# Optimization experiments

Hardware: AMD Instinct MI355X
Metric: run time of the kernel (lower is better)

The kernel has to match this reference:

```python
import jax, jax.numpy as jnp
import numpy as np

B, N, H, E = 4, 256, 128, 16
EIN = 2 * H + 1 + E  # edge MLP input dim
LN_EPS = 1e-6  # flax nnx.LayerNorm default epsilon


def layer_norm(x, scale, bias):
    m = jnp.mean(x, axis=-1, keepdims=True)
    v = jnp.var(x, axis=-1, keepdims=True)
    return (x - m) * jax.lax.rsqrt(v + LN_EPS) * scale + bias


def mlp2(x, W1, b1, s, sb, W2, b2):
    # Linear -> LayerNorm -> ReLU -> Linear (dropout deterministic)
    h = jax.nn.relu(layer_norm(x @ W1 + b1, s, sb))
    return h @ W2 + b2


def setup_inputs() -> dict:
    key = jax.random.key(0)
    ks = jax.random.split(key, 24)

    def lin(k, fi, fo):
        k1, k2 = jax.random.split(k)
        W = jax.random.normal(k1, (fi, fo), jnp.float32) / np.sqrt(fi)
        b = jnp.zeros((fo,), jnp.float32)
        return W, b

    We1, be1 = lin(ks[0], EIN, H)
    We2, be2 = lin(ks[1], H, H)
    Wa, ba = lin(ks[2], EIN, 1)
    Wn1, bn1 = lin(ks[3], 2 * H, H)
    Wn2, bn2 = lin(ks[4], H, H)
    Wc1, bc1 = lin(ks[5], H, H)
    Wc2, bc2 = lin(ks[6], H, 1)

    return {
        "node_features": jax.random.normal(ks[7], (B, N, H), jnp.float32),
        "coordinates": jax.random.normal(ks[8], (B, N, 3), jnp.float32),
        "edge_features": jax.random.normal(ks[9], (B, N, N, E), jnp.float32),
        "mask": jnp.ones((B, N), jnp.float32),
        "We1": We1, "be1": be1,
        "ln_e_s": jnp.ones((H,), jnp.float32), "ln_e_b": jnp.zeros((H,), jnp.float32),
        "We2": We2, "be2": be2,
        "Wa": Wa, "ba": ba,
        "Wn1": Wn1, "bn1": bn1,
        "ln_n_s": jnp.ones((H,), jnp.float32), "ln_n_b": jnp.zeros((H,), jnp.float32),
        "Wn2": Wn2, "bn2": bn2,
        "Wc1": Wc1, "bc1": bc1,
        "ln_c_s": jnp.ones((H,), jnp.float32), "ln_c_b": jnp.zeros((H,), jnp.float32),
        "Wc2": Wc2, "bc2": bc2,
        "edge_index": jax.random.randint(ks[10], (B, N, N), 0, 2, jnp.int32),
    }


def reference(node_features, coordinates, edge_features, mask,
              We1, be1, ln_e_s, ln_e_b, We2, be2,
              Wa, ba,
              Wn1, bn1, ln_n_s, ln_n_b, Wn2, bn2,
              Wc1, bc1, ln_c_s, ln_c_b, Wc2, bc2,
              edge_index):
    b, n, h = node_features.shape
    rel_pos = coordinates[:, :, None, :] - coordinates[:, None, :, :]  # [B,N,N,3]
    d2 = jnp.sum(rel_pos ** 2, axis=-1, keepdims=True)                 # [B,N,N,1]

    node_i = jnp.broadcast_to(node_features[:, :, None, :], (b, n, n, h))
    node_j = jnp.broadcast_to(node_features[:, None, :, :], (b, n, n, h))
    edge_inputs = jnp.concatenate([node_i, node_j, d2, edge_features], axis=-1)  # [B,N,N,EIN]

    edge_messages = mlp2(edge_inputs, We1, be1, ln_e_s, ln_e_b, We2, be2)  # [B,N,N,H]
    new_edge_features = edge_messages

    att = jax.nn.sigmoid(edge_inputs @ Wa + ba)  # [B,N,N,1]
    adj = edge_index[..., None].astype(edge_messages.dtype)  # [B,N,N,1]
    msg_mask = (mask[:, :, None] * mask[:, None, :])[..., None]

    edge_messages = edge_messages * att * adj * msg_mask
    node_messages = jnp.sum(edge_messages, axis=2)  # [B,N,H]

    node_inputs = jnp.concatenate([node_features, node_messages], axis=-1)
    new_node_features = mlp2(node_inputs, Wn1, bn1, ln_n_s, ln_n_b, Wn2, bn2)

    coord_messages = mlp2(node_messages, Wc1, bc1, ln_c_s, ln_c_b, Wc2, bc2)  # [B,N,1]

    norm = jnp.sqrt(d2 + 1e-8)
    normalized_rel_pos = rel_pos / norm
    coord_update_dir = jnp.sum(normalized_rel_pos * att * adj, axis=2)  # [B,N,3]
    coord_updates = coord_update_dir * coord_messages * mask[:, :, None]
    new_coordinates = coordinates + coord_updates

    new_node_features = node_features + new_node_features  # residual
    return (new_node_features, new_coordinates, new_edge_features)
```

## Files before the change

kernel.cpp:

```cpp
#include <hip/hip_runtime.h>
#include <hip/hip_bf16.h>


typedef unsigned short ushort_t;
typedef __attribute__((ext_vector_type(8))) short short8;
typedef __attribute__((ext_vector_type(4))) float f32x4;

__device__ __forceinline__ ushort_t f2bf(float f) {
  unsigned int x = __builtin_bit_cast(unsigned int, f);
  x += 0x7fffu + ((x >> 16) & 1u);
  return (ushort_t)(x >> 16);
}

__global__ void k_sent777(float* out0) { out0[threadIdx.x] = 777.f; }

__global__ __launch_bounds__(128)
void k_pre(const float* nf, const float* We1, const float* be1,
           const float* Wa, float* pre_i, float* pre_j, float* api, float* apj) {
  int r = blockIdx.x, t = threadIdx.x;
  __shared__ float nfv[128];
  __shared__ float red[4];
  nfv[t] = nf[(size_t)r * 128 + t];
  __syncthreads();
  float s1 = be1[t], s2 = 0.f;
  for (int c = 0; c < 128; ++c) {
    float x = nfv[c];
    s1 += x * We1[c * 128 + t];
    s2 += x * We1[(128 + c) * 128 + t];
  }
  pre_i[(size_t)r * 128 + t] = s1;
  pre_j[(size_t)r * 128 + t] = s2;
  float t1 = nfv[t] * Wa[t];
  float t2 = nfv[t] * Wa[128 + t];
#pragma unroll
  for (int o = 32; o > 0; o >>= 1) { t1 += __shfl_down(t1, o); t2 += __shfl_down(t2, o); }
  if ((t & 63) == 0) { red[(t >> 6) * 2] = t1; red[(t >> 6) * 2 + 1] = t2; }
  __syncthreads();
  if (t == 0) { api[r] = red[0] + red[2]; apj[r] = red[1] + red[3]; }
}

__global__ __launch_bounds__(256)
void k_pack(const float* We2, ushort_t* bpack) {
  int t = blockIdx.x * 256 + threadIdx.x;
  if (t >= 2048) return;
  int ks = t >> 9, nt = (t >> 6) & 7, l = t & 63;
  int kb = ks * 32 + (l >> 4) * 8, col = nt * 16 + (l & 15);
#pragma unroll
  for (int e = 0; e < 8; ++e) bpack[t * 8 + e] = f2bf(We2[(kb + e) * 128 + col]);
}

__global__ __launch_bounds__(256)
void k_edge(const float* co, const float* efo, const float* mk,
            const float* We1, const float* be2, const float* Wa, const float* ba,
            const float* lnes, const float* lneb, const int* eidx,
            const float* pre_i, const float* pre_j, const float* api, const float* apj,
            const ushort_t* bpack, float* oute, float* nm2, float* cd2) {
  __shared__ __align__(16) ushort_t h1s[128 * 136];
  __shared__ float wef[17 * 128];
  __shared__ float lns[128], lnb[128];
  __shared__ float attw[128];
  __shared__ float lnS[256], lnSS[256];
  __shared__ float nmp[4][128];
  __shared__ float cred[2][3];

  const int bx = blockIdx.x;
  const int r = bx >> 1, half = bx & 1;
  const int b = r >> 8;
  const int t = threadIdx.x;
  const int lane = t & 63, w = t >> 6;

  for (int q = t; q < 17 * 128; q += 256) {
    int e = q >> 7, c = q & 127;
    int row = (e < 16) ? (257 + e) : 256;
    wef[q] = We1[row * 128 + c];
  }
  if (t < 128) { lns[t] = lnes[t]; }
  else { lnb[t - 128] = lneb[t - 128]; }
  __syncthreads();

  const int jr = t & 127, ch = t >> 7;
  const int j = half * 128 + jr;
  const int gj = b * 256 + j;

  float dx = co[r * 3 + 0] - co[gj * 3 + 0];
  float dy = co[r * 3 + 1] - co[gj * 3 + 1];
  float dz = co[r * 3 + 2] - co[gj * 3 + 2];
  float d2 = dx * dx + dy * dy + dz * dz;

  float efv[17];
  {
    const float* efp = efo + ((size_t)r * 256 + j) * 16;
    f32x4 e0 = *reinterpret_cast<const f32x4*>(efp);
    f32x4 e1 = *reinterpret_cast<const f32x4*>(efp + 4);
    f32x4 e2 = *reinterpret_cast<const f32x4*>(efp + 8);
    f32x4 e3 = *reinterpret_cast<const f32x4*>(efp + 12);
#pragma unroll
    for (int x = 0; x < 4; ++x) {
      efv[x] = e0[x]; efv[4 + x] = e1[x]; efv[8 + x] = e2[x]; efv[12 + x] = e3[x];
    }
  }
  efv[16] = d2;

  if (ch == 0) {
    float a = api[r] + apj[gj] + ba[0] + d2 * Wa[256];
#pragma unroll
    for (int e = 0; e < 16; ++e) a += efv[e] * Wa[257 + e];
    float att = 1.f / (1.f + __expf(-a));
    float aw = att * (float)eidx[(size_t)r * 256 + j];
    attw[jr] = aw * mk[r] * mk[gj];
    float invn = rsqrtf(d2 + 1e-8f);
    float c0 = dx * invn * aw, c1 = dy * invn * aw, c2 = dz * invn * aw;
#pragma unroll
    for (int o = 32; o > 0; o >>= 1) {
      c0 += __shfl_down(c0, o); c1 += __shfl_down(c1, o); c2 += __shfl_down(c2, o);
    }
    if (lane == 0) { cred[w][0] = c0; cred[w][1] = c1; cred[w][2] = c2; }
  }

  const int cbase = ch * 64;
  const f32x4* pi4 = reinterpret_cast<const f32x4*>(pre_i + (size_t)r * 128 + cbase);
  const f32x4* pj4 = reinterpret_cast<const f32x4*>(pre_j + (size_t)gj * 128 + cbase);
  const f32x4* wef4 = reinterpret_cast<const f32x4*>(wef);
  float h[64];
  float s = 0.f, ss = 0.f;
#pragma unroll
  for (int c4 = 0; c4 < 16; ++c4) {
    f32x4 v = pi4[c4] + pj4[c4];
#pragma unroll
    for (int e = 0; e < 17; ++e) v += efv[e] * wef4[e * 32 + (cbase >> 2) + c4];
#pragma unroll
    for (int x = 0; x < 4; ++x) { h[c4 * 4 + x] = v[x]; s += v[x]; ss += v[x] * v[x]; }
  }
  lnS[t] = s; lnSS[t] = ss;
  __syncthreads();
  float st = s + lnS[t ^ 128], sst = ss + lnSS[t ^ 128];
  float mean = st * (1.f / 128.f);
  float var = fmaxf(sst * (1.f / 128.f) - mean * mean, 0.f);
  float rsv = rsqrtf(var + 1e-6f);
  ushort_t* hrow = h1s + jr * 136 + cbase;
#pragma unroll
  for (int q8 = 0; q8 < 8; ++q8) {
    short8 pk;
#pragma unroll
    for (int x = 0; x < 8; ++x) {
      int c = q8 * 8 + x;
      float gv = (h[c] - mean) * rsv * lns[cbase + c] + lnb[cbase + c];
      pk[x] = (short)f2bf(fmaxf(gv, 0.f));
    }
    *reinterpret_cast<short8*>(hrow + q8 * 8) = pk;
  }
  __syncthreads();

  if (t == 0) {
#pragma unroll
    for (int d = 0; d < 3; ++d)
      cd2[(size_t)(half * 1024 + r) * 3 + d] = cred[0][d] + cred[1][d];
  }

  f32x4 acc[2][8];
#pragma unroll
  for (int mt = 0; mt < 2; ++mt)
#pragma unroll
    for (int nt = 0; nt < 8; ++nt) acc[mt][nt] = (f32x4){0.f, 0.f, 0.f, 0.f};

  const short* h1p = reinterpret_cast<const short*>(h1s);
#pragma unroll
  for (int ks = 0; ks < 4; ++ks) {
    short8 bfr[8];
#pragma unroll
    for (int nt = 0; nt < 8; ++nt)
      bfr[nt] = *reinterpret_cast<const short8*>(bpack + (((ks * 8 + nt) * 64 + lane) * 8));
#pragma unroll
    for (int mt = 0; mt < 2; ++mt) {
      short8 afr = *reinterpret_cast<const short8*>(
          h1p + (w * 32 + mt * 16 + (lane & 15)) * 136 + ks * 32 + ((lane >> 4) * 8));
#pragma unroll
      for (int nt = 0; nt < 8; ++nt)
        acc[mt][nt] = __builtin_amdgcn_mfma_f32_16x16x32_bf16(afr, bfr[nt], acc[mt][nt], 0, 0, 0);
    }
  }

  float be2v[8], pnm[8];
#pragma unroll
  for (int nt = 0; nt < 8; ++nt) { be2v[nt] = be2[nt * 16 + (lane & 15)]; pnm[nt] = 0.f; }
  const size_t obase = ((size_t)r * 256 + half * 128) * 128;
#pragma unroll
  for (int mt = 0; mt < 2; ++mt)
#pragma unroll
    for (int r4 = 0; r4 < 4; ++r4) {
      int row = w * 32 + mt * 16 + (lane >> 4) * 4 + r4;
      float wgt = attw[row];
#pragma unroll
      for (int nt = 0; nt < 8; ++nt) {
        float val = acc[mt][nt][r4] + be2v[nt];
        oute[obase + (size_t)row * 128 + nt * 16 + (lane & 15)] = val;
        pnm[nt] += val * wgt;
      }
    }
#pragma unroll
  for (int nt = 0; nt < 8; ++nt) {
    pnm[nt] += __shfl_xor(pnm[nt], 16);
    pnm[nt] += __shfl_xor(pnm[nt], 32);
  }
  if (lane < 16)
#pragma unroll
    for (int nt = 0; nt < 8; ++nt) nmp[w][nt * 16 + lane] = pnm[nt];
  __syncthreads();
  if (t < 128)
    nm2[(size_t)(half * 1024 + r) * 128 + t] = nmp[0][t] + nmp[1][t] + nmp[2][t] + nmp[3][t];
}

__device__ __forceinline__ float bsum128(float v, float* red, int t) {
#pragma unroll
  for (int o = 32; o > 0; o >>= 1) v += __shfl_down(v, o);
  __syncthreads();
  if ((t & 63) == 0) red[t >> 6] = v;
  __syncthreads();
  return red[0] + red[1];
}

__global__ __launch_bounds__(128)
void k_node(const float* nf, const float* co, const float* mk,
            const float* Wn1, const float* bn1, const float* lnns, const float* lnnb,
            const float* Wn2, const float* bn2,
            const float* Wc1, const float* bc1, const float* lncs, const float* lncb,
            const float* Wc2, const float* bc2,
            const float* nm2, const float* cd2,
            float* out0, float* out1) {
  int r = blockIdx.x, t = threadIdx.x;
  __shared__ float nin[256];
  __shared__ float hf[128];
  __shared__ float red[2];
  float nfv = nf[(size_t)r * 128 + t];
  float nmv = nm2[(size_t)r * 128 + t] + nm2[(size_t)(1024 + r) * 128 + t];
  nin[t] = nfv; nin[128 + t] = nmv;
  __syncthreads();
  float s1 = bn1[t];
  for (int c = 0; c < 256; ++c) s1 += nin[c] * Wn1[c * 128 + t];
  float mean = bsum128(s1, red, t) * (1.f / 128.f);
  float var = fmaxf(bsum128(s1 * s1, red, t) * (1.f / 128.f) - mean * mean, 0.f);
  float hv = (s1 - mean) * rsqrtf(var + 1e-6f) * lnns[t] + lnnb[t];
  hv = fmaxf(hv, 0.f);
  hf[t] = hv;
  __syncthreads();
  float o1 = bn2[t] + nfv;
  for (int c = 0; c < 128; ++c) o1 += hf[c] * Wn2[c * 128 + t];
  out0[(size_t)r * 128 + t] = o1;
  float g = bc1[t];
  for (int c = 0; c < 128; ++c) g += nin[128 + c] * Wc1[c * 128 + t];
  float gm = bsum128(g, red, t) * (1.f / 128.f);
  float gv = fmaxf(bsum128(g * g, red, t) * (1.f / 128.f) - gm * gm, 0.f);
  float gh = fmaxf((g - gm) * rsqrtf(gv + 1e-6f) * lncs[t] + lncb[t], 0.f);
  float cm = bsum128(gh * Wc2[t], red, t) + bc2[0];
  if (t < 3) {
    float cd = cd2[(size_t)r * 3 + t] + cd2[(size_t)(1024 + r) * 3 + t];
    float nc = co[(size_t)r * 3 + t] + cd * cm * mk[r];
    out1[(size_t)r * 3 + t] = nc;
  }
}

extern "C" void kernel_launch(void* const* d_in, const int* in_sizes, int n_in,
                              void* d_out, int out_size, void* d_ws, size_t ws_size,
                              hipStream_t stream) {
  const float* nf   = (const float*)d_in[0];
  const float* co   = (const float*)d_in[1];
  const float* efo  = (const float*)d_in[2];
  const float* mk   = (const float*)d_in[3];
  const float* We1  = (const float*)d_in[4];
  const float* be1  = (const float*)d_in[5];
  const float* lnes = (const float*)d_in[6];
  const float* lneb = (const float*)d_in[7];
  const float* We2  = (const float*)d_in[8];
  const float* be2  = (const float*)d_in[9];
  const float* Wa   = (const float*)d_in[10];
  const float* ba   = (const float*)d_in[11];
  const float* Wn1  = (const float*)d_in[12];
  const float* bn1  = (const float*)d_in[13];
  const float* lnns = (const float*)d_in[14];
  const float* lnnb = (const float*)d_in[15];
  const float* Wn2  = (const float*)d_in[16];
  const float* bn2  = (const float*)d_in[17];
  const float* Wc1  = (const float*)d_in[18];
  const float* bc1  = (const float*)d_in[19];
  const float* lncs = (const float*)d_in[20];
  const float* lncb = (const float*)d_in[21];
  const float* Wc2  = (const float*)d_in[22];
  const float* bc2  = (const float*)d_in[23];
  const int* eidx   = (const int*)d_in[24];

  float* out0 = (float*)d_out;
  float* out1 = out0 + 131072;
  float* oute = out1 + 3072;

  const size_t need = (size_t)(131072 + 131072 + 1024 + 1024 + 262144 + 6144) * 4 + 16384 * 2;
  if (ws_size < need) {
    k_sent777<<<1, 128, 0, stream>>>(out0);
    return;
  }
  float* ws    = (float*)d_ws;
  float* pre_i = ws;
  float* pre_j = pre_i + 131072;
  float* api   = pre_j + 131072;
  float* apj   = api + 1024;
  float* nm2   = apj + 1024;
  float* cd2   = nm2 + 262144;
  ushort_t* bpack = (ushort_t*)(cd2 + 6144);

  k_pre<<<1024, 128, 0, stream>>>(nf, We1, be1, Wa, pre_i, pre_j, api, apj);
  k_pack<<<8, 256, 0, stream>>>(We2, bpack);
  k_edge<<<2048, 256, 0, stream>>>(co, efo, mk, We1, be2, Wa, ba, lnes, lneb, eidx,
                                   pre_i, pre_j, api, apj, bpack, oute, nm2, cd2);
  k_node<<<1024, 128, 0, stream>>>(nf, co, mk, Wn1, bn1, lnns, lnnb, Wn2, bn2,
                                   Wc1, bc1, lncs, lncb, Wc2, bc2, nm2, cd2, out0, out1);
}
```

Baseline: 93.02 us.

## Double edge-kernel threads and transpose MFMA operands for vectorized stores

The edge kernel now runs 512 threads per block, so each thread handles 32 hidden channels of the first layer instead of 64, and LayerNorm statistics are combined across four partial sums. The second-layer MFMA swaps operands: packed We2 becomes the A fragment and the hidden rows become the B fragment, one 16-row tile per wave. Each lane then holds four consecutive output columns, which allows 128-bit stores and a shuffle-based reduction over rows for the node messages. The aim is more latency hiding and wider stores, but the launch bound requesting four blocks per CU caps registers per thread, which risks spills, and LDS usage may still limit how many blocks actually reside.

```diff
diff --git a/kernel.cpp b/kernel.cpp
--- a/kernel.cpp
+++ b/kernel.cpp
@@ -43,13 +43,13 @@
 void k_pack(const float* We2, ushort_t* bpack) {
   int t = blockIdx.x * 256 + threadIdx.x;
   if (t >= 2048) return;
-  int ks = t >> 9, nt = (t >> 6) & 7, l = t & 63;
-  int kb = ks * 32 + (l >> 4) * 8, col = nt * 16 + (l & 15);
+  int ks = t >> 9, mt = (t >> 6) & 7, l = t & 63;
+  int kb = ks * 32 + (l >> 4) * 8, col = mt * 16 + (l & 15);
 #pragma unroll
   for (int e = 0; e < 8; ++e) bpack[t * 8 + e] = f2bf(We2[(kb + e) * 128 + col]);
 }
 
-__global__ __launch_bounds__(256)
+__global__ __launch_bounds__(512, 4)
 void k_edge(const float* co, const float* efo, const float* mk,
             const float* We1, const float* be2, const float* Wa, const float* ba,
             const float* lnes, const float* lneb, const int* eidx,
@@ -59,8 +59,8 @@
   __shared__ float wef[17 * 128];
   __shared__ float lns[128], lnb[128];
   __shared__ float attw[128];
-  __shared__ float lnS[256], lnSS[256];
-  __shared__ float nmp[4][128];
+  __shared__ float lnS[512], lnSS[512];
+  __shared__ float nmp[8][128];
   __shared__ float cred[2][3];
 
   const int bx = blockIdx.x;
@@ -69,13 +69,13 @@
   const int t = threadIdx.x;
   const int lane = t & 63, w = t >> 6;
 
-  for (int q = t; q < 17 * 128; q += 256) {
+  for (int q = t; q < 17 * 128; q += 512) {
     int e = q >> 7, c = q & 127;
     int row = (e < 16) ? (257 + e) : 256;
     wef[q] = We1[row * 128 + c];
   }
   if (t < 128) { lns[t] = lnes[t]; }
-  else { lnb[t - 128] = lneb[t - 128]; }
+  else if (t < 256) { lnb[t - 128] = lneb[t - 128]; }
   __syncthreads();
 
   const int jr = t & 127, ch = t >> 7;
@@ -117,14 +117,14 @@
     if (lane == 0) { cred[w][0] = c0; cred[w][1] = c1; cred[w][2] = c2; }
   }
 
-  const int cbase = ch * 64;
+  const int cbase = ch * 32;
   const f32x4* pi4 = reinterpret_cast<const f32x4*>(pre_i + (size_t)r * 128 + cbase);
   const f32x4* pj4 = reinterpret_cast<const f32x4*>(pre_j + (size_t)gj * 128 + cbase);
   const f32x4* wef4 = reinterpret_cast<const f32x4*>(wef);
-  float h[64];
+  float h[32];
   float s = 0.f, ss = 0.f;
 #pragma unroll
-  for (int c4 = 0; c4 < 16; ++c4) {
+  for (int c4 = 0; c4 < 8; ++c4) {
     f32x4 v = pi4[c4] + pj4[c4];
 #pragma unroll
     for (int e = 0; e < 17; ++e) v += efv[e] * wef4[e * 32 + (cbase >> 2) + c4];
@@ -133,13 +133,14 @@
   }
   lnS[t] = s; lnSS[t] = ss;
   __syncthreads();
-  float st = s + lnS[t ^ 128], sst = ss + lnSS[t ^ 128];
+  float st  = lnS[jr] + lnS[jr + 128] + lnS[jr + 256] + lnS[jr + 384];
+  float sst = lnSS[jr] + lnSS[jr + 128] + lnSS[jr + 256] + lnSS[jr + 384];
   float mean = st * (1.f / 128.f);
   float var = fmaxf(sst * (1.f / 128.f) - mean * mean, 0.f);
   float rsv = rsqrtf(var + 1e-6f);
   ushort_t* hrow = h1s + jr * 136 + cbase;
 #pragma unroll
-  for (int q8 = 0; q8 < 8; ++q8) {
+  for (int q8 = 0; q8 < 4; ++q8) {
     short8 pk;
 #pragma unroll
     for (int x = 0; x < 8; ++x) {
@@ -157,57 +158,56 @@
       cd2[(size_t)(half * 1024 + r) * 3 + d] = cred[0][d] + cred[1][d];
   }
 
-  f32x4 acc[2][8];
-#pragma unroll
-  for (int mt = 0; mt < 2; ++mt)
-#pragma unroll
-    for (int nt = 0; nt < 8; ++nt) acc[mt][nt] = (f32x4){0.f, 0.f, 0.f, 0.f};
+  f32x4 acc[8];
+#pragma unroll
+  for (int mt = 0; mt < 8; ++mt) acc[mt] = (f32x4){0.f, 0.f, 0.f, 0.f};
 
   const short* h1p = reinterpret_cast<const short*>(h1s);
+  const int nrow = w * 16 + (lane & 15);
 #pragma unroll
   for (int ks = 0; ks < 4; ++ks) {
-    short8 bfr[8];
-#pragma unroll
-    for (int nt = 0; nt < 8; ++nt)
-      bfr[nt] = *reinterpret_cast<const short8*>(bpack + (((ks * 8 + nt) * 64 + lane) * 8));
-#pragma unroll
-    for (int mt = 0; mt < 2; ++mt) {
-      short8 afr = *reinterpret_cast<const short8*>(
-          h1p + (w * 32 + mt * 16 + (lane & 15)) * 136 + ks * 32 + ((lane >> 4) * 8));
-#pragma unroll
-      for (int nt = 0; nt < 8; ++nt)
-        acc[mt][nt] = __builtin_amdgcn_mfma_f32_16x16x32_bf16(afr, bfr[nt], acc[mt][nt], 0, 0, 0);
-    }
-  }
-
-  float be2v[8], pnm[8];
-#pragma unroll
-  for (int nt = 0; nt < 8; ++nt) { be2v[nt] = be2[nt * 16 + (lane & 15)]; pnm[nt] = 0.f; }
+    short8 hfr = *reinterpret_cast<const short8*>(
+        h1p + nrow * 136 + ks * 32 + ((lane >> 4) * 8));
+#pragma unroll
+    for (int mt = 0; mt < 8; ++mt) {
+      short8 afr = *reinterpret_cast<const short8*>(bpack + (((ks * 8 + mt) * 64 + lane) * 8));
+      acc[mt] = __builtin_amdgcn_mfma_f32_16x16x32_bf16(afr, hfr, acc[mt], 0, 0, 0);
+    }
+  }
+
   const size_t obase = ((size_t)r * 256 + half * 128) * 128;
-#pragma unroll
-  for (int mt = 0; mt < 2; ++mt)
-#pragma unroll
-    for (int r4 = 0; r4 < 4; ++r4) {
-      int row = w * 32 + mt * 16 + (lane >> 4) * 4 + r4;
-      float wgt = attw[row];
-#pragma unroll
-      for (int nt = 0; nt < 8; ++nt) {
-        float val = acc[mt][nt][r4] + be2v[nt];
-        oute[obase + (size_t)row * 128 + nt * 16 + (lane & 15)] = val;
-        pnm[nt] += val * wgt;
-      }
-    }
-#pragma unroll
-  for (int nt = 0; nt < 8; ++nt) {
-    pnm[nt] += __shfl_xor(pnm[nt], 16);
-    pnm[nt] += __shfl_xor(pnm[nt], 32);
-  }
-  if (lane < 16)
-#pragma unroll
-    for (int nt = 0; nt < 8; ++nt) nmp[w][nt * 16 + lane] = pnm[nt];
-  __syncthreads();
-  if (t < 128)
-    nm2[(size_t)(half * 1024 + r) * 128 + t] = nmp[0][t] + nmp[1][t] + nmp[2][t] + nmp[3][t];
+  const float wgt = attw[nrow];
+  const int mq = (lane >> 4) * 4;
+  float pm[8][4];
+#pragma unroll
+  for (int mt = 0; mt < 8; ++mt) {
+    f32x4 b4 = *reinterpret_cast<const f32x4*>(be2 + mt * 16 + mq);
+    f32x4 val = acc[mt] + b4;
+    *reinterpret_cast<f32x4*>(oute + obase + (size_t)nrow * 128 + mt * 16 + mq) = val;
+#pragma unroll
+    for (int x = 0; x < 4; ++x) pm[mt][x] = val[x] * wgt;
+  }
+#pragma unroll
+  for (int mt = 0; mt < 8; ++mt)
+#pragma unroll
+    for (int x = 0; x < 4; ++x) {
+      float v = pm[mt][x];
+      v += __shfl_xor(v, 1); v += __shfl_xor(v, 2);
+      v += __shfl_xor(v, 4); v += __shfl_xor(v, 8);
+      pm[mt][x] = v;
+    }
+  if ((lane & 15) == 0) {
+#pragma unroll
+    for (int mt = 0; mt < 8; ++mt)
+#pragma unroll
+      for (int x = 0; x < 4; ++x) nmp[w][mt * 16 + mq + x] = pm[mt][x];
+  }
+  __syncthreads();
+  if (t < 128) {
+    float acc8 = nmp[0][t] + nmp[1][t] + nmp[2][t] + nmp[3][t]
+               + nmp[4][t] + nmp[5][t] + nmp[6][t] + nmp[7][t];
+    nm2[(size_t)(half * 1024 + r) * 128 + t] = acc8;
+  }
 }
 
 __device__ __forceinline__ float bsum128(float v, float* red, int t) {
@@ -308,7 +308,7 @@
 
   k_pre<<<1024, 128, 0, stream>>>(nf, We1, be1, Wa, pre_i, pre_j, api, apj);
   k_pack<<<8, 256, 0, stream>>>(We2, bpack);
-  k_edge<<<2048, 256, 0, stream>>>(co, efo, mk, We1, be2, Wa, ba, lnes, lneb, eidx,
+  k_edge<<<2048, 512, 0, stream>>>(co, efo, mk, We1, be2, Wa, ba, lnes, lneb, eidx,
                                    pre_i, pre_j, api, apj, bpack, oute, nm2, cd2);
   k_node<<<1024, 128, 0, stream>>>(nf, co, mk, Wn1, bn1, lnns, lnnb, Wn2, bn2,
                                    Wc1, bc1, lncs, lncb, Wc2, bc2, nm2, cd2, out0, out1);
```

After: 114.3 us. 1.23x slower.
